# Kernel tuning notes

Hardware: AMD Instinct MI355X
Metric: run time of the kernel (lower is better)

The kernel has to match this reference:

```python
import jax, jax.numpy as jnp
import numpy as np
from jax import lax

# Static pair index table: all C(135,2)=9045 unordered node pairs (replaces the
# nested Python loops with a single gather).
PAIR_I, PAIR_J = np.triu_indices(135, k=1)
RRELU_SLOPE = (1.0 / 8.0 + 1.0 / 3.0) / 2.0  # eval-mode RReLU negative slope
BN_SCALE = 1.0 / float(np.sqrt(1.0 + 1e-5))  # eval BN with running mean=0, var=1


def _leaky(x):
    return jnp.where(x > 0, x, 0.01 * x)


def _conv1d(x, w, b):
    # x: (N, Cin, L), w: (Cout, Cin, K) -> (N, Cout, L-K+1), VALID
    y = lax.conv_general_dilated(x, w, (1,), 'VALID',
                                 dimension_numbers=('NCH', 'OIH', 'NCH'))
    return y + b[None, :, None]


def _bn_eval(x, g, b):
    # nn.BatchNorm1d in eval with fresh running stats (mean=0, var=1)
    return x * (g * BN_SCALE)[None, :, None] + b[None, :, None]


def _maxpool2d(x):
    # nn.MaxPool2d(2) applied to a 3D (N, H, W) tensor: 2x2 pool over (H, W)
    return lax.reduce_window(x, -jnp.inf, lax.max, (1, 2, 2), (1, 2, 2), 'VALID')


def setup_inputs() -> dict:
    key = jax.random.key(0)
    ks = iter(jax.random.split(key, 40))

    def w(shape, scale=0.05):
        return (jax.random.normal(next(ks), shape, jnp.float32) * scale)

    inp = {
        'x': jax.random.normal(next(ks), (30, 135, 375), jnp.float32),
        # FeatureExtractor
        'conv1_w': w((32, 1, 3)), 'conv1_b': jnp.zeros((32,), jnp.float32),
        'bn1_g': jnp.ones((32,), jnp.float32), 'bn1_b': jnp.zeros((32,), jnp.float32),
        'conv2_w': w((64, 16, 3)), 'conv2_b': jnp.zeros((64,), jnp.float32),
        'bn2_g': jnp.ones((64,), jnp.float32), 'bn2_b': jnp.zeros((64,), jnp.float32),
        'conv3_w': w((96, 32, 3)), 'conv3_b': jnp.zeros((96,), jnp.float32),
        'bn3_g': jnp.ones((96,), jnp.float32), 'bn3_b': jnp.zeros((96,), jnp.float32),
        'fe_fc_w': w((48 * 45, 32)), 'fe_fc_b': jnp.zeros((32,), jnp.float32),
        # SimilarityMeasureNetwork
        'sim_w1': w((64, 32)), 'sim_b1': jnp.zeros((32,), jnp.float32),
        'sim_w2': w((32, 16)), 'sim_b2': jnp.zeros((16,), jnp.float32),
        'sim_w3': w((16, 8)), 'sim_b3': jnp.zeros((8,), jnp.float32),
        'sim_w4': w((8, 1)), 'sim_b4': jnp.zeros((1,), jnp.float32),
        # ClassificationNet(9045, 3)
        'cls_w1': w((9045, 1024), 0.01), 'cls_b1': jnp.zeros((1024,), jnp.float32),
        'cls_w2': w((1024, 256)), 'cls_b2': jnp.zeros((256,), jnp.float32),
        'cls_w3': w((256, 64)), 'cls_b3': jnp.zeros((64,), jnp.float32),
        'cls_w4': w((64, 3)), 'cls_b4': jnp.zeros((3,), jnp.float32),
    }
    return inp


def reference(x, conv1_w, conv1_b, bn1_g, bn1_b, conv2_w, conv2_b, bn2_g, bn2_b,
              conv3_w, conv3_b, bn3_g, bn3_b, fe_fc_w, fe_fc_b,
              sim_w1, sim_b1, sim_w2, sim_b2, sim_w3, sim_b3, sim_w4, sim_b4,
              cls_w1, cls_b1, cls_w2, cls_b2, cls_w3, cls_b3, cls_w4, cls_b4):
    B = x.shape[0]  # 30 subjects
    h = x.reshape(B * 135, 1, 375)
    # FeatureExtractor (all subjects*nodes batched together)
    h = _maxpool2d(_leaky(_bn_eval(_conv1d(h, conv1_w, conv1_b), bn1_g, bn1_b)))  # (N,16,186)
    h = _maxpool2d(_leaky(_bn_eval(_conv1d(h, conv2_w, conv2_b), bn2_g, bn2_b)))  # (N,32,92)
    h = _maxpool2d(_leaky(_bn_eval(_conv1d(h, conv3_w, conv3_b), bn3_g, bn3_b)))  # (N,48,45)
    h = h.reshape(B * 135, -1) @ fe_fc_w + fe_fc_b  # (B*135, 32)
    feats = h.reshape(B, 135, 32)

    # All-pairs concat: single gather replacing the nested loops -> (B, 9045, 64)
    pi = jnp.asarray(PAIR_I)
    pj = jnp.asarray(PAIR_J)
    pairs = jnp.concatenate([feats[:, pi, :], feats[:, pj, :]], axis=-1)

    # SimilarityMeasureNetwork
    s = jax.nn.relu(pairs @ sim_w1 + sim_b1)
    s = jax.nn.relu(s @ sim_w2 + sim_b2)
    s = jax.nn.relu(s @ sim_w3 + sim_b3)
    s = jnp.tanh(s @ sim_w4 + sim_b4)  # (B, 9045, 1)
    subjects = s[..., 0]  # (B, 9045)

    # ClassificationNet (eval mode: RReLU -> fixed slope, dropout -> identity)
    c = subjects @ cls_w1 + cls_b1
    c = jnp.where(c >= 0, c, RRELU_SLOPE * c)
    c = jax.nn.relu(c @ cls_w2 + cls_b2)
    c = jax.nn.relu(c @ cls_w3 + cls_b3)
    c = c @ cls_w4 + cls_b4
    return jax.nn.log_softmax(c, axis=1)  # (B, 3)
```

## Files before the change

kernel.cpp:

```cpp
#include <hip/hip_runtime.h>
#include <math.h>

#define BN_SCALE 0.99999500003749967f
#define RRELU_SLOPE 0.22916666666666666f

static __device__ __forceinline__ float leaky(float v) { return v > 0.f ? v : 0.01f * v; }

typedef __attribute__((ext_vector_type(8))) short bf16x8;
typedef __attribute__((ext_vector_type(4))) float f32x4;

static __device__ __forceinline__ unsigned short f2bf(float f) {
  unsigned u = __builtin_bit_cast(unsigned, f);
  u = (u + 0x7FFFu + ((u >> 16) & 1u)) >> 16;
  return (unsigned short)u;
}

__global__ __launch_bounds__(256) void setup_kernel(
    const float* __restrict__ w2c, const float* __restrict__ g2,
    const float* __restrict__ w3c, const float* __restrict__ g3,
    const float* __restrict__ fcw, const float* __restrict__ fcb,
    const float* __restrict__ w1,  const float* __restrict__ b1,
    const float* __restrict__ cw1,
    unsigned short* __restrict__ w2frag,
    unsigned short* __restrict__ w3frag,
    unsigned short* __restrict__ bfragGG,
    float* __restrict__ bgagb,
    unsigned short* __restrict__ subjectsA,
    unsigned short* __restrict__ w1T)
{
  __shared__ float tile[64][65];
  const int t = threadIdx.x;
  if (blockIdx.x < 2272) {
    const int kt = blockIdx.x >> 4;
    const int ntb = blockIdx.x & 15;
    const int k0 = kt * 64, n0 = ntb * 64;
#pragma unroll 4
    for (int i = 0; i < 16; ++i) {
      const int idx = i * 256 + t;
      const int kk = idx >> 6, nn = idx & 63;
      const int k = k0 + kk;
      tile[kk][nn] = (k < 9045) ? cw1[(size_t)k * 1024 + n0 + nn] : 0.f;
    }
    __syncthreads();
#pragma unroll 4
    for (int i = 0; i < 8; ++i) {
      const int idx = i * 256 + t;
      const int nn = idx >> 5;
      const int kp = (idx & 31) * 2;
      const unsigned lo = f2bf(tile[kp][nn]);
      const unsigned hi = f2bf(tile[kp + 1][nn]);
      ((unsigned*)w1T)[(size_t)(n0 + nn) * 4544 + (k0 >> 1) + (idx & 31)] = lo | (hi << 16);
    }
    return;
  }
  const int item = (blockIdx.x - 2272) * 256 + t;
  if (item < 512) {
    const int tl = item >> 6, lane = item & 63;
    const int mt = tl >> 1, kc = tl & 1;
    const int lr = lane & 15, quad = lane >> 4;
    const int c = mt * 16 + lr;
    const float gs = g2[c] * BN_SCALE;
#pragma unroll
    for (int j = 0; j < 8; ++j) {
      const int k = quad * 8 + j;
      float v;
      if (kc == 0) { const int tap = k >> 4, ci = k & 15; v = w2c[c * 48 + ci * 3 + tap] * gs; }
      else         { v = (k < 16) ? w2c[c * 48 + k * 3 + 2] * gs : 0.f; }
      w2frag[item * 8 + j] = f2bf(v);
    }
  } else if (item < 1664) {
    const int it = item - 512;
    const int tl = it >> 6, lane = it & 63;
    const int mt = tl / 3, tap = tl - mt * 3;
    const int lr = lane & 15, quad = lane >> 4;
    const int c = mt * 16 + lr;
    const float gs = g3[c] * BN_SCALE;
#pragma unroll
    for (int j = 0; j < 8; ++j) {
      const int ci = quad * 8 + j;
      w3frag[it * 8 + j] = f2bf(w3c[c * 96 + ci * 3 + tap] * gs);
    }
  } else if (item < 19072) {
    const int it = item - 1664;
    const int chunk = it >> 8;
    const int rem = it & 255;
    const int nt = rem >> 6;
    const int lane = rem & 63;
    const int lr = lane & 15, quad = lane >> 4;
    const int n = nt * 16 + lr;
    const int off = (n >= 32) ? 32 : 0;
    const int nj = n & 31;
    float w1col[32];
#pragma unroll 8
    for (int q = 0; q < 32; ++q) w1col[q] = w1[(q + off) * 32 + nj];
#pragma unroll
    for (int j = 0; j < 8; ++j) {
      const int k = chunk * 32 + quad * 8 + j;
      float v = 0.f;
      if (k < 2160) {
        const float* fr = fcw + (size_t)k * 32;
#pragma unroll 8
        for (int q = 0; q < 32; ++q) v = fmaf(fr[q], w1col[q], v);
      }
      bfragGG[(size_t)it * 8 + j] = f2bf(v);
    }
  } else if (item < 19136) {
    const int n = item - 19072;
    const int off = (n >= 32) ? 32 : 0;
    const int nj = n & 31;
    float s = (n < 32) ? b1[nj] : 0.f;
    for (int q = 0; q < 32; ++q) s = fmaf(fcb[q], w1[(q + off) * 32 + nj], s);
    bgagb[n] = s;
  } else if (item < 55360) {
    const int idx = item - 19136;
    uint4 z = {0u, 0u, 0u, 0u};
    ((uint4*)subjectsA)[idx] = z;
  }
}

__global__ __launch_bounds__(128) void fe_kernel(
    const float* __restrict__ x,
    const float* __restrict__ w1c, const float* __restrict__ b1c,
    const float* __restrict__ g1,  const float* __restrict__ bb1,
    const float* __restrict__ b2c, const float* __restrict__ g2, const float* __restrict__ bb2,
    const float* __restrict__ b3c, const float* __restrict__ g3, const float* __restrict__ bb3,
    const unsigned short* __restrict__ w2frag,
    const unsigned short* __restrict__ w3frag,
    unsigned short* __restrict__ act3)
{
  __shared__ __align__(16) char smem[2 * 6912];
  const int t = threadIdx.x;
  const int wv = t >> 6, lane = t & 63, quad = lane >> 4, lr = lane & 15;
  const int n = blockIdx.x * 2 + wv;

  char* A = smem + wv * 6912;
  unsigned short* buf = (unsigned short*)A;
  float* be2 = (float*)(A + 6272);
  float* be3 = (float*)(A + 6528);

  bf16x8 a2[4][2];
#pragma unroll
  for (int mt = 0; mt < 4; ++mt)
#pragma unroll
    for (int kc = 0; kc < 2; ++kc)
      a2[mt][kc] = *(const bf16x8*)(w2frag + ((mt * 2 + kc) * 64 + lane) * 8);

  be2[lane] = b2c[lane] * (g2[lane] * BN_SCALE) + bb2[lane];
  be3[lane] = b3c[lane] * (g3[lane] * BN_SCALE) + bb3[lane];
  if (lane < 32) be3[64 + lane] = b3c[64 + lane] * (g3[64 + lane] * BN_SCALE) + bb3[64 + lane];
  ((unsigned*)buf)[1488 + lane] = 0;

  const int cp = lane & 7;
  float u[4][3], bbr[4];
#pragma unroll
  for (int d = 0; d < 4; ++d) {
    const int c = cp * 4 + d;
    const float gs = g1[c] * BN_SCALE;
    u[d][0] = w1c[c * 3 + 0] * gs;
    u[d][1] = w1c[c * 3 + 1] * gs;
    u[d][2] = w1c[c * 3 + 2] * gs;
    bbr[d] = b1c[c] * gs + bb1[c];
  }

  const float* xr = x + (size_t)n * 375;
  for (int o = lane; o < 1488; o += 64) {
    const int l = o >> 3;
    const int p = 2 * l;
    const float x0 = xr[p], x1 = xr[p + 1], x2 = xr[p + 2], x3 = xr[p + 3];
    unsigned pk = 0;
#pragma unroll
    for (int uu = 0; uu < 2; ++uu) {
      float m = -3.4e38f;
#pragma unroll
      for (int dc = 0; dc < 2; ++dc) {
        const int d = uu * 2 + dc;
        const float v0 = fmaf(x0, u[d][0], fmaf(x1, u[d][1], fmaf(x2, u[d][2], bbr[d])));
        const float v1 = fmaf(x1, u[d][0], fmaf(x2, u[d][1], fmaf(x3, u[d][2], bbr[d])));
        m = fmaxf(m, fmaxf(leaky(v0), leaky(v1)));
      }
      pk |= (unsigned)f2bf(m) << (16 * uu);
    }
    ((unsigned*)buf)[l * 8 + cp] = pk;
  }

  float be2r[4][4];
#pragma unroll
  for (int mt = 0; mt < 4; ++mt)
#pragma unroll
    for (int r = 0; r < 4; ++r) be2r[mt][r] = be2[mt * 16 + quad * 4 + r];

#pragma unroll 2
  for (int nt = 0; nt < 12; ++nt) {
    const int nrow = nt * 16 + lr;
    bf16x8 b0 = *(const bf16x8*)(buf + (nrow + (quad >> 1)) * 16 + (quad & 1) * 8);
    bf16x8 b1 = *(const bf16x8*)(buf + (nrow + 2) * 16 + (quad & 1) * 8);
    f32x4 acc[4];
#pragma unroll
    for (int mt = 0; mt < 4; ++mt)
#pragma unroll
      for (int r = 0; r < 4; ++r) acc[mt][r] = be2r[mt][r];
#pragma unroll
    for (int mt = 0; mt < 4; ++mt)
      acc[mt] = __builtin_amdgcn_mfma_f32_16x16x32_bf16(a2[mt][0], b0, acc[mt], 0, 0, 0);
#pragma unroll
    for (int mt = 0; mt < 4; ++mt)
      acc[mt] = __builtin_amdgcn_mfma_f32_16x16x32_bf16(a2[mt][1], b1, acc[mt], 0, 0, 0);
#pragma unroll
    for (int mt = 0; mt < 4; ++mt) {
      float o[4];
#pragma unroll
      for (int r = 0; r < 4; ++r) {
        const float v = leaky(acc[mt][r]);
        o[r] = fmaxf(v, __shfl_xor(v, 1));
      }
      if ((lr & 1) == 0) {
        const int np = nrow >> 1;
        if (np <= 91) {
          const float m0 = fmaxf(o[0], o[1]);
          const float m1 = fmaxf(o[2], o[3]);
          const unsigned pk = (unsigned)f2bf(m0) | ((unsigned)f2bf(m1) << 16);
          ((unsigned*)buf)[np * 16 + mt * 4 + quad] = pk;
        }
      }
    }
  }

  ((unsigned*)buf)[1472 + lane] = 0;
  if (lane < 32) ((unsigned*)buf)[1536 + lane] = 0;

  unsigned short* actr = act3 + (size_t)n * 2176;
  for (int mt = 0; mt < 6; ++mt) {
    bf16x8 a3[3];
#pragma unroll
    for (int tap = 0; tap < 3; ++tap)
      a3[tap] = *(const bf16x8*)(w3frag + ((mt * 3 + tap) * 64 + lane) * 8);
    float be3r[4];
#pragma unroll
    for (int r = 0; r < 4; ++r) be3r[r] = be3[mt * 16 + quad * 4 + r];
#pragma unroll
    for (int nt = 0; nt < 6; ++nt) {
      const int nrow = nt * 16 + lr;
      f32x4 acc;
#pragma unroll
      for (int r = 0; r < 4; ++r) acc[r] = be3r[r];
#pragma unroll
      for (int tap = 0; tap < 3; ++tap) {
        bf16x8 b = *(const bf16x8*)(buf + (nrow + tap) * 32 + quad * 8);
        acc = __builtin_amdgcn_mfma_f32_16x16x32_bf16(a3[tap], b, acc, 0, 0, 0);
      }
      float o[4];
#pragma unroll
      for (int r = 0; r < 4; ++r) {
        const float v = leaky(acc[r]);
        o[r] = fmaxf(v, __shfl_xor(v, 1));
      }
      if ((lr & 1) == 0) {
        const int np = nrow >> 1;
        if (np <= 44) {
          const int mp = mt * 8 + quad * 2;
          actr[mp * 45 + np] = f2bf(fmaxf(o[0], o[1]));
          actr[(mp + 1) * 45 + np] = f2bf(fmaxf(o[2], o[3]));
        }
      }
    }
  }
  if (lane < 16) actr[2160 + lane] = 0;
}

__global__ __launch_bounds__(256) void gagb_kernel(
    const unsigned short* __restrict__ act3,
    const unsigned short* __restrict__ bfragGG,
    const float* __restrict__ bgagb,
    float* __restrict__ Ga, float* __restrict__ Gb)
{
  __shared__ f32x4 sred[3][4][64];
  const int t = threadIdx.x;
  const int wv = t >> 6, lane = t & 63, quad = lane >> 4, lr = lane & 15;
  const int m0 = blockIdx.x * 16;
  const int arow = min(m0 + lr, 4049);

  f32x4 acc[4] = {};
  const int c0 = wv * 17;
  for (int chunk = c0; chunk < c0 + 17; ++chunk) {
    const bf16x8 a = *(const bf16x8*)(act3 + (size_t)arow * 2176 + chunk * 32 + quad * 8);
#pragma unroll
    for (int nt = 0; nt < 4; ++nt) {
      const bf16x8 b = *(const bf16x8*)(bfragGG + ((size_t)(chunk * 4 + nt) * 64 + lane) * 8);
      acc[nt] = __builtin_amdgcn_mfma_f32_16x16x32_bf16(a, b, acc[nt], 0, 0, 0);
    }
  }
  if (wv > 0) {
#pragma unroll
    for (int nt = 0; nt < 4; ++nt) sred[wv - 1][nt][lane] = acc[nt];
  }
  __syncthreads();
  if (wv == 0) {
#pragma unroll
    for (int nt = 0; nt < 4; ++nt) {
      f32x4 s = acc[nt];
#pragma unroll
      for (int q = 0; q < 3; ++q) {
        const f32x4 o = sred[q][nt][lane];
#pragma unroll
        for (int r = 0; r < 4; ++r) s[r] += o[r];
      }
      const int col = nt * 16 + lr;
      const float bias = bgagb[col];
#pragma unroll
      for (int r = 0; r < 4; ++r) {
        const int row = m0 + quad * 4 + r;
        if (row < 4050) {
          const float v = s[r] + bias;
          if (col < 32) Ga[row * 32 + col] = v;
          else          Gb[row * 32 + (col - 32)] = v;
        }
      }
    }
  }
}

__global__ __launch_bounds__(256) void sim_kernel(
    const float* __restrict__ Ga, const float* __restrict__ Gb,
    const float* __restrict__ w2, const float* __restrict__ b2,
    const float* __restrict__ w3, const float* __restrict__ b3,
    const float* __restrict__ w4, const float* __restrict__ b4,
    unsigned short* __restrict__ subjectsA)
{
  __shared__ float sGa[135 * 36];
  __shared__ float sGb[135 * 36];
  __shared__ float sw2[512], sw3[128], sw4[8];
  __shared__ float sb2[16], sb3[8], sb4v[1];

  const int t = threadIdx.x;
  const int b = blockIdx.x >> 5;
  const int c = blockIdx.x & 31;

  for (int i = t; i < 4320; i += 256) {
    const int r = i >> 5, col = i & 31;
    sGa[r * 36 + col] = Ga[b * 4320 + i];
    sGb[r * 36 + col] = Gb[b * 4320 + i];
  }
  for (int i = t; i < 512; i += 256) sw2[i] = w2[i];
  if (t < 128) sw3[t] = w3[t];
  if (t < 8) sw4[t] = w4[t];
  if (t < 16) sb2[t] = b2[t];
  if (t < 8) sb3[t] = b3[t];
  if (t == 0) sb4v[0] = b4[0];
  __syncthreads();

  const int mtile = b >> 4, lrm = b & 15;
  const int pend = min(9045, (c + 1) * 283);
  for (int p = c * 283 + t; p < pend; p += 256) {
    int i = (int)((269.0f - sqrtf((float)(72361 - 8 * p))) * 0.5f);
    i = max(0, min(133, i));
    while (134 * (i + 1) - ((i + 1) * i) / 2 <= p) ++i;
    while (134 * i - (i * (i - 1)) / 2 > p) --i;
    const int j = i + 1 + (p - (134 * i - (i * (i - 1)) / 2));

    float h1[32];
#pragma unroll
    for (int q = 0; q < 8; ++q) {
      const float4 va = *(const float4*)(&sGa[i * 36 + 4 * q]);
      const float4 vb = *(const float4*)(&sGb[j * 36 + 4 * q]);
      h1[4 * q + 0] = fmaxf(va.x + vb.x, 0.f);
      h1[4 * q + 1] = fmaxf(va.y + vb.y, 0.f);
      h1[4 * q + 2] = fmaxf(va.z + vb.z, 0.f);
      h1[4 * q + 3] = fmaxf(va.w + vb.w, 0.f);
    }

    float h2[16];
#pragma unroll
    for (int jj = 0; jj < 16; ++jj) h2[jj] = sb2[jj];
#pragma unroll 8
    for (int ii = 0; ii < 32; ++ii) {
      const float av = h1[ii];
      const float4* wr = reinterpret_cast<const float4*>(&sw2[ii * 16]);
#pragma unroll
      for (int r = 0; r < 4; ++r) {
        float4 w = wr[r];
        h2[4 * r + 0] = fmaf(av, w.x, h2[4 * r + 0]);
        h2[4 * r + 1] = fmaf(av, w.y, h2[4 * r + 1]);
        h2[4 * r + 2] = fmaf(av, w.z, h2[4 * r + 2]);
        h2[4 * r + 3] = fmaf(av, w.w, h2[4 * r + 3]);
      }
    }
#pragma unroll
    for (int jj = 0; jj < 16; ++jj) h2[jj] = fmaxf(h2[jj], 0.f);

    float h3[8];
#pragma unroll
    for (int jj = 0; jj < 8; ++jj) h3[jj] = sb3[jj];
#pragma unroll
    for (int ii = 0; ii < 16; ++ii) {
      const float av = h2[ii];
      const float4* wr = reinterpret_cast<const float4*>(&sw3[ii * 8]);
#pragma unroll
      for (int r = 0; r < 2; ++r) {
        float4 w = wr[r];
        h3[4 * r + 0] = fmaf(av, w.x, h3[4 * r + 0]);
        h3[4 * r + 1] = fmaf(av, w.y, h3[4 * r + 1]);
        h3[4 * r + 2] = fmaf(av, w.z, h3[4 * r + 2]);
        h3[4 * r + 3] = fmaf(av, w.w, h3[4 * r + 3]);
      }
    }
#pragma unroll
    for (int jj = 0; jj < 8; ++jj) h3[jj] = fmaxf(h3[jj], 0.f);

    float z = sb4v[0];
#pragma unroll
    for (int ii = 0; ii < 8; ++ii) z = fmaf(h3[ii], sw4[ii], z);

    const float az = fabsf(z);
    const float e = __expf(-2.f * az);
    const float rr = (1.f - e) / (1.f + e);
    const float val = copysignf(rr, z);

    const int chunk = p >> 5, q8 = (p & 31) >> 3, jj2 = p & 7;
    subjectsA[chunk * 1024 + mtile * 512 + (q8 * 16 + lrm) * 8 + jj2] = f2bf(val);
  }
}

__global__ __launch_bounds__(256) void c1_kernel(
    const unsigned short* __restrict__ subjectsA,
    const unsigned short* __restrict__ w1T,
    float* __restrict__ part)
{
  const int t = threadIdx.x;
  const int wv = t >> 6, lane = t & 63, quad = lane >> 4, lr = lane & 15;
  const int job = blockIdx.x * 4 + wv;
  const int ng = job & 15;
  const int kg = job >> 4;
  const int c0 = kg * 5;
  const int cend = min(283, c0 + 5);

  f32x4 acc[2][4] = {};
  for (int ch = c0; ch < cend; ++ch) {
    const bf16x8 a0 = *(const bf16x8*)(subjectsA + ch * 1024 + lane * 8);
    const bf16x8 a1 = *(const bf16x8*)(subjectsA + ch * 1024 + 512 + lane * 8);
#pragma unroll
    for (int nt = 0; nt < 4; ++nt) {
      const int col = (ng * 4 + nt) * 16 + lr;
      const bf16x8 b = *(const bf16x8*)(w1T + (size_t)col * 9088 + ch * 32 + quad * 8);
      acc[0][nt] = __builtin_amdgcn_mfma_f32_16x16x32_bf16(a0, b, acc[0][nt], 0, 0, 0);
      acc[1][nt] = __builtin_amdgcn_mfma_f32_16x16x32_bf16(a1, b, acc[1][nt], 0, 0, 0);
    }
  }
#pragma unroll
  for (int mt = 0; mt < 2; ++mt)
#pragma unroll
    for (int r = 0; r < 4; ++r) {
      const int m = mt * 16 + quad * 4 + r;
      if (m < 30) {
#pragma unroll
        for (int nt = 0; nt < 4; ++nt) {
          const int col = (ng * 4 + nt) * 16 + lr;
          part[(size_t)(m * 64 + kg) * 1024 + col] = acc[mt][nt][r];
        }
      }
    }
}

__global__ __launch_bounds__(256) void tail_a_kernel(
    const float* __restrict__ part,
    const float* __restrict__ cb1,
    float* __restrict__ act1)
{
  const int r = blockIdx.x >> 2;
  const int cg = blockIdx.x & 3;
  const int j = cg * 256 + threadIdx.x;
  float s = cb1[j];
  const float* pp = part + (size_t)r * 64 * 1024 + j;
#pragma unroll 8
  for (int q = 0; q < 64; ++q) s += pp[q * 1024];
  act1[r * 1024 + j] = s >= 0.f ? s : RRELU_SLOPE * s;
}

__global__ __launch_bounds__(256) void tail_b_kernel(
    const float* __restrict__ act1,
    const float* __restrict__ w2, const float* __restrict__ cb2,
    float* __restrict__ act2)
{
  __shared__ float sa[1024];
  __shared__ float sp[256];
  const int r = blockIdx.x >> 3;
  const int cg = blockIdx.x & 7;
  const int t = threadIdx.x;
  const int c = t & 31;
  const int ks = t >> 5;
  const int col = cg * 32 + c;

  for (int i = t; i < 1024; i += 256) sa[i] = act1[r * 1024 + i];
  __syncthreads();

  float acc = 0.f;
  const int k0 = ks * 128;
  for (int kk = k0; kk < k0 + 128; kk += 4) {
    const float4 a = *reinterpret_cast<const float4*>(&sa[kk]);
    acc = fmaf(a.x, w2[(kk + 0) * 256 + col], acc);
    acc = fmaf(a.y, w2[(kk + 1) * 256 + col], acc);
    acc = fmaf(a.z, w2[(kk + 2) * 256 + col], acc);
    acc = fmaf(a.w, w2[(kk + 3) * 256 + col], acc);
  }
  sp[t] = acc;
  __syncthreads();
  if (t < 32) {
    float s = cb2[col];
#pragma unroll
    for (int q = 0; q < 8; ++q) s += sp[q * 32 + t];
    act2[r * 256 + cg * 32 + t] = fmaxf(s, 0.f);
  }
}

__global__ __launch_bounds__(256) void tail_c_kernel(
    const float* __restrict__ act2,
    const float* __restrict__ w3, const float* __restrict__ cb3,
    const float* __restrict__ w4, const float* __restrict__ cb4,
    float* __restrict__ out)
{
  __shared__ float sa[256];
  __shared__ float sp[256];
  __shared__ float sc3[64];
  __shared__ float slg[3];
  const int r = blockIdx.x, t = threadIdx.x;
  const int c = t & 63;
  const int ks = t >> 6;

  sa[t] = act2[r * 256 + t];
  __syncthreads();
  {
    float acc = 0.f;
    const int k0 = ks * 64;
#pragma unroll 4
    for (int kk = k0; kk < k0 + 64; ++kk)
      acc = fmaf(sa[kk], w3[kk * 64 + c], acc);
    sp[t] = acc;
  }
  __syncthreads();
  if (t < 64) {
    const float s = cb3[t] + sp[t] + sp[t + 64] + sp[t + 128] + sp[t + 192];
    sc3[t] = fmaxf(s, 0.f);
  }
  __syncthreads();
  if (t < 3) {
    float acc = cb4[t];
#pragma unroll
    for (int kk = 0; kk < 64; ++kk) acc = fmaf(sc3[kk], w4[kk * 3 + t], acc);
    slg[t] = acc;
  }
  __syncthreads();
  if (t == 0) {
    float m = fmaxf(slg[0], fmaxf(slg[1], slg[2]));
    float se = __expf(slg[0] - m) + __expf(slg[1] - m) + __expf(slg[2] - m);
    float lse = m + logf(se);
    out[r * 3 + 0] = slg[0] - lse;
    out[r * 3 + 1] = slg[1] - lse;
    out[r * 3 + 2] = slg[2] - lse;
  }
}

extern "C" void kernel_launch(void* const* d_in, const int* in_sizes, int n_in,
                              void* d_out, int out_size, void* d_ws, size_t ws_size,
                              hipStream_t stream) {
  const float* x    = (const float*)d_in[0];
  const float* w1c  = (const float*)d_in[1];
  const float* b1c  = (const float*)d_in[2];
  const float* g1   = (const float*)d_in[3];
  const float* bb1  = (const float*)d_in[4];
  const float* w2c  = (const float*)d_in[5];
  const float* b2c  = (const float*)d_in[6];
  const float* g2   = (const float*)d_in[7];
  const float* bb2  = (const float*)d_in[8];
  const float* w3c  = (const float*)d_in[9];
  const float* b3c  = (const float*)d_in[10];
  const float* g3   = (const float*)d_in[11];
  const float* bb3  = (const float*)d_in[12];
  const float* fcw  = (const float*)d_in[13];
  const float* fcb  = (const float*)d_in[14];
  const float* sw1  = (const float*)d_in[15];
  const float* sb1  = (const float*)d_in[16];
  const float* sw2  = (const float*)d_in[17];
  const float* sb2  = (const float*)d_in[18];
  const float* sw3  = (const float*)d_in[19];
  const float* sb3  = (const float*)d_in[20];
  const float* sw4  = (const float*)d_in[21];
  const float* sb4  = (const float*)d_in[22];
  const float* cw1  = (const float*)d_in[23];
  const float* cb1  = (const float*)d_in[24];
  const float* cw2  = (const float*)d_in[25];
  const float* cb2  = (const float*)d_in[26];
  const float* cw3  = (const float*)d_in[27];
  const float* cb3  = (const float*)d_in[28];
  const float* cw4  = (const float*)d_in[29];
  const float* cb4  = (const float*)d_in[30];

  float* ws = (float*)d_ws;
  float* Ga    = ws;
  float* Gb    = ws + 129600;
  float* part  = ws + 259200;
  float* bgagb = ws + 2225280;
  float* act1  = ws + 2225344;
  float* act2  = ws + 2256064;
  unsigned short* wsu = (unsigned short*)(ws + 2263744);
  unsigned short* w2frag    = wsu;
  unsigned short* w3frag    = wsu + 4096;
  unsigned short* bfragGG   = wsu + 13312;
  unsigned short* act3      = wsu + 152576;
  unsigned short* subjectsA = wsu + 8965376;
  unsigned short* w1T       = wsu + 9255168;

  setup_kernel<<<2489, 256, 0, stream>>>(w2c, g2, w3c, g3, fcw, fcb, sw1, sb1, cw1,
                                         w2frag, w3frag, bfragGG, bgagb, subjectsA, w1T);
  fe_kernel<<<2025, 128, 0, stream>>>(x, w1c, b1c, g1, bb1, b2c, g2, bb2,
                                      b3c, g3, bb3, w2frag, w3frag, act3);
  gagb_kernel<<<254, 256, 0, stream>>>(act3, bfragGG, bgagb, Ga, Gb);
  sim_kernel<<<960, 256, 0, stream>>>(Ga, Gb, sw2, sb2, sw3, sb3, sw4, sb4, subjectsA);
  c1_kernel<<<256, 256, 0, stream>>>(subjectsA, w1T, part);
  tail_a_kernel<<<120, 256, 0, stream>>>(part, cb1, act1);
  tail_b_kernel<<<240, 256, 0, stream>>>(act1, cw2, cb2, act2);
  tail_c_kernel<<<30, 256, 0, stream>>>(act2, cw3, cb3, cw4, cb4, (float*)d_out);
}
```

Measured before the change: 270.5 us.

## Merge setup and feature extractor, atomically reduce classifier partials, fuse tail kernels

New measurement: 315.6 us. 16.7% more time.

```diff
diff --git a/kernel.cpp b/kernel.cpp
--- a/kernel.cpp
+++ b/kernel.cpp
@@ -15,24 +15,194 @@
   return (unsigned short)u;
 }
 
-__global__ __launch_bounds__(256) void setup_kernel(
-    const float* __restrict__ w2c, const float* __restrict__ g2,
-    const float* __restrict__ w3c, const float* __restrict__ g3,
+__global__ __launch_bounds__(256) void big_kernel(
+    const float* __restrict__ x,
+    const float* __restrict__ w1c, const float* __restrict__ b1c,
+    const float* __restrict__ g1,  const float* __restrict__ bb1,
+    const float* __restrict__ w2c, const float* __restrict__ b2c,
+    const float* __restrict__ g2,  const float* __restrict__ bb2,
+    const float* __restrict__ w3c, const float* __restrict__ b3c,
+    const float* __restrict__ g3,  const float* __restrict__ bb3,
     const float* __restrict__ fcw, const float* __restrict__ fcb,
     const float* __restrict__ w1,  const float* __restrict__ b1,
-    const float* __restrict__ cw1,
-    unsigned short* __restrict__ w2frag,
-    unsigned short* __restrict__ w3frag,
+    const float* __restrict__ cw1, const float* __restrict__ cb1,
+    unsigned short* __restrict__ act3,
     unsigned short* __restrict__ bfragGG,
     float* __restrict__ bgagb,
     unsigned short* __restrict__ subjectsA,
-    unsigned short* __restrict__ w1T)
+    unsigned short* __restrict__ w1T,
+    float* __restrict__ act1pre)
 {
-  __shared__ float tile[64][65];
+  __shared__ __align__(16) char smem[27648];
   const int t = threadIdx.x;
-  if (blockIdx.x < 2272) {
-    const int kt = blockIdx.x >> 4;
-    const int ntb = blockIdx.x & 15;
+
+  if (blockIdx.x < 1013) {
+    const int wv = t >> 6, lane = t & 63, quad = lane >> 4, lr = lane & 15;
+    const int n = blockIdx.x * 4 + wv;
+    if (n >= 4050) return;
+
+    char* A = smem + wv * 6912;
+    unsigned short* buf = (unsigned short*)A;
+    float* be2 = (float*)(A + 6272);
+    float* be3 = (float*)(A + 6528);
+
+    bf16x8 a2[4][2];
+#pragma unroll
+    for (int mt = 0; mt < 4; ++mt) {
+      const int c = mt * 16 + lr;
+      const float gs = g2[c] * BN_SCALE;
+#pragma unroll
+      for (int kc = 0; kc < 2; ++kc) {
+        bf16x8 fr;
+#pragma unroll
+        for (int j = 0; j < 8; ++j) {
+          const int k = quad * 8 + j;
+          float v;
+          if (kc == 0) { const int tap = k >> 4, ci = k & 15; v = w2c[c * 48 + ci * 3 + tap] * gs; }
+          else         { v = (k < 16) ? w2c[c * 48 + k * 3 + 2] * gs : 0.f; }
+          fr[j] = (short)f2bf(v);
+        }
+        a2[mt][kc] = fr;
+      }
+    }
+
+    be2[lane] = b2c[lane] * (g2[lane] * BN_SCALE) + bb2[lane];
+    be3[lane] = b3c[lane] * (g3[lane] * BN_SCALE) + bb3[lane];
+    if (lane < 32) be3[64 + lane] = b3c[64 + lane] * (g3[64 + lane] * BN_SCALE) + bb3[64 + lane];
+    ((unsigned*)buf)[1488 + lane] = 0;
+
+    const int cp = lane & 7;
+    float u[4][3], bbr[4];
+#pragma unroll
+    for (int d = 0; d < 4; ++d) {
+      const int c = cp * 4 + d;
+      const float gs = g1[c] * BN_SCALE;
+      u[d][0] = w1c[c * 3 + 0] * gs;
+      u[d][1] = w1c[c * 3 + 1] * gs;
+      u[d][2] = w1c[c * 3 + 2] * gs;
+      bbr[d] = b1c[c] * gs + bb1[c];
+    }
+
+    const float* xr = x + (size_t)n * 375;
+    for (int o = lane; o < 1488; o += 64) {
+      const int l = o >> 3;
+      const int p = 2 * l;
+      const float x0 = xr[p], x1 = xr[p + 1], x2 = xr[p + 2], x3 = xr[p + 3];
+      unsigned pk = 0;
+#pragma unroll
+      for (int uu = 0; uu < 2; ++uu) {
+        float m = -3.4e38f;
+#pragma unroll
+        for (int dc = 0; dc < 2; ++dc) {
+          const int d = uu * 2 + dc;
+          const float v0 = fmaf(x0, u[d][0], fmaf(x1, u[d][1], fmaf(x2, u[d][2], bbr[d])));
+          const float v1 = fmaf(x1, u[d][0], fmaf(x2, u[d][1], fmaf(x3, u[d][2], bbr[d])));
+          m = fmaxf(m, fmaxf(leaky(v0), leaky(v1)));
+        }
+        pk |= (unsigned)f2bf(m) << (16 * uu);
+      }
+      ((unsigned*)buf)[l * 8 + cp] = pk;
+    }
+
+    float be2r[4][4];
+#pragma unroll
+    for (int mt = 0; mt < 4; ++mt)
+#pragma unroll
+      for (int r = 0; r < 4; ++r) be2r[mt][r] = be2[mt * 16 + quad * 4 + r];
+
+#pragma unroll 2
+    for (int nt = 0; nt < 12; ++nt) {
+      const int nrow = nt * 16 + lr;
+      bf16x8 b0 = *(const bf16x8*)(buf + (nrow + (quad >> 1)) * 16 + (quad & 1) * 8);
+      bf16x8 b1 = *(const bf16x8*)(buf + (nrow + 2) * 16 + (quad & 1) * 8);
+      f32x4 acc[4];
+#pragma unroll
+      for (int mt = 0; mt < 4; ++mt)
+#pragma unroll
+        for (int r = 0; r < 4; ++r) acc[mt][r] = be2r[mt][r];
+#pragma unroll
+      for (int mt = 0; mt < 4; ++mt)
+        acc[mt] = __builtin_amdgcn_mfma_f32_16x16x32_bf16(a2[mt][0], b0, acc[mt], 0, 0, 0);
+#pragma unroll
+      for (int mt = 0; mt < 4; ++mt)
+        acc[mt] = __builtin_amdgcn_mfma_f32_16x16x32_bf16(a2[mt][1], b1, acc[mt], 0, 0, 0);
+#pragma unroll
+      for (int mt = 0; mt < 4; ++mt) {
+        float o[4];
+#pragma unroll
+        for (int r = 0; r < 4; ++r) {
+          const float v = leaky(acc[mt][r]);
+          o[r] = fmaxf(v, __shfl_xor(v, 1));
+        }
+        if ((lr & 1) == 0) {
+          const int np = nrow >> 1;
+          if (np <= 91) {
+            const float m0 = fmaxf(o[0], o[1]);
+            const float m1 = fmaxf(o[2], o[3]);
+            const unsigned pk = (unsigned)f2bf(m0) | ((unsigned)f2bf(m1) << 16);
+            ((unsigned*)buf)[np * 16 + mt * 4 + quad] = pk;
+          }
+        }
+      }
+    }
+
+    ((unsigned*)buf)[1472 + lane] = 0;
+    if (lane < 32) ((unsigned*)buf)[1536 + lane] = 0;
+
+    unsigned short* actr = act3 + (size_t)n * 2176;
+    for (int mt = 0; mt < 6; ++mt) {
+      const int c = mt * 16 + lr;
+      const float gs3v = g3[c] * BN_SCALE;
+      bf16x8 a3[3];
+#pragma unroll
+      for (int tap = 0; tap < 3; ++tap) {
+        bf16x8 fr;
+#pragma unroll
+        for (int j = 0; j < 8; ++j) {
+          const int ci = quad * 8 + j;
+          fr[j] = (short)f2bf(w3c[c * 96 + ci * 3 + tap] * gs3v);
+        }
+        a3[tap] = fr;
+      }
+      float be3r[4];
+#pragma unroll
+      for (int r = 0; r < 4; ++r) be3r[r] = be3[mt * 16 + quad * 4 + r];
+#pragma unroll
+      for (int nt = 0; nt < 6; ++nt) {
+        const int nrow = nt * 16 + lr;
+        f32x4 acc;
+#pragma unroll
+        for (int r = 0; r < 4; ++r) acc[r] = be3r[r];
+#pragma unroll
+        for (int tap = 0; tap < 3; ++tap) {
+          bf16x8 b = *(const bf16x8*)(buf + (nrow + tap) * 32 + quad * 8);
+          acc = __builtin_amdgcn_mfma_f32_16x16x32_bf16(a3[tap], b, acc, 0, 0, 0);
+        }
+        float o[4];
+#pragma unroll
+        for (int r = 0; r < 4; ++r) {
+          const float v = leaky(acc[r]);
+          o[r] = fmaxf(v, __shfl_xor(v, 1));
+        }
+        if ((lr & 1) == 0) {
+          const int np = nrow >> 1;
+          if (np <= 44) {
+            const int mp = mt * 8 + quad * 2;
+            actr[mp * 45 + np] = f2bf(fmaxf(o[0], o[1]));
+            actr[(mp + 1) * 45 + np] = f2bf(fmaxf(o[2], o[3]));
+          }
+        }
+      }
+    }
+    if (lane < 16) actr[2160 + lane] = 0;
+    return;
+  }
+
+  const int sb = blockIdx.x - 1013;
+  if (sb < 2272) {
+    float (*tile)[65] = (float(*)[65])smem;
+    const int kt = sb >> 4;
+    const int ntb = sb & 15;
     const int k0 = kt * 64, n0 = ntb * 64;
 #pragma unroll 4
     for (int i = 0; i < 16; ++i) {
@@ -53,43 +223,17 @@
     }
     return;
   }
-  const int item = (blockIdx.x - 2272) * 256 + t;
-  if (item < 512) {
-    const int tl = item >> 6, lane = item & 63;
-    const int mt = tl >> 1, kc = tl & 1;
-    const int lr = lane & 15, quad = lane >> 4;
-    const int c = mt * 16 + lr;
-    const float gs = g2[c] * BN_SCALE;
-#pragma unroll
-    for (int j = 0; j < 8; ++j) {
-      const int k = quad * 8 + j;
-      float v;
-      if (kc == 0) { const int tap = k >> 4, ci = k & 15; v = w2c[c * 48 + ci * 3 + tap] * gs; }
-      else         { v = (k < 16) ? w2c[c * 48 + k * 3 + 2] * gs : 0.f; }
-      w2frag[item * 8 + j] = f2bf(v);
-    }
-  } else if (item < 1664) {
-    const int it = item - 512;
-    const int tl = it >> 6, lane = it & 63;
-    const int mt = tl / 3, tap = tl - mt * 3;
-    const int lr = lane & 15, quad = lane >> 4;
-    const int c = mt * 16 + lr;
-    const float gs = g3[c] * BN_SCALE;
-#pragma unroll
-    for (int j = 0; j < 8; ++j) {
-      const int ci = quad * 8 + j;
-      w3frag[it * 8 + j] = f2bf(w3c[c * 96 + ci * 3 + tap] * gs);
-    }
-  } else if (item < 19072) {
-    const int it = item - 1664;
-    const int chunk = it >> 8;
-    const int rem = it & 255;
+
+  const int item = (sb - 2272) * 256 + t;
+  if (item < 17408) {
+    const int chunk = item >> 8;
+    const int rem = item & 255;
     const int nt = rem >> 6;
     const int lane = rem & 63;
     const int lr = lane & 15, quad = lane >> 4;
-    const int n = nt * 16 + lr;
-    const int off = (n >= 32) ? 32 : 0;
-    const int nj = n & 31;
+    const int nn = nt * 16 + lr;
+    const int off = (nn >= 32) ? 32 : 0;
+    const int nj = nn & 31;
     float w1col[32];
 #pragma unroll 8
     for (int q = 0; q < 32; ++q) w1col[q] = w1[(q + off) * 32 + nj];
@@ -102,169 +246,25 @@
 #pragma unroll 8
         for (int q = 0; q < 32; ++q) v = fmaf(fr[q], w1col[q], v);
       }
-      bfragGG[(size_t)it * 8 + j] = f2bf(v);
-    }
-  } else if (item < 19136) {
-    const int n = item - 19072;
-    const int off = (n >= 32) ? 32 : 0;
-    const int nj = n & 31;
-    float s = (n < 32) ? b1[nj] : 0.f;
+      bfragGG[(size_t)item * 8 + j] = f2bf(v);
+    }
+  } else if (item < 17472) {
+    const int nn = item - 17408;
+    const int off = (nn >= 32) ? 32 : 0;
+    const int nj = nn & 31;
+    float s = (nn < 32) ? b1[nj] : 0.f;
     for (int q = 0; q < 32; ++q) s = fmaf(fcb[q], w1[(q + off) * 32 + nj], s);
-    bgagb[n] = s;
-  } else if (item < 55360) {
-    const int idx = item - 19136;
+    bgagb[nn] = s;
+  } else if (item < 53696) {
+    const int idx = item - 17472;
     uint4 z = {0u, 0u, 0u, 0u};
     ((uint4*)subjectsA)[idx] = z;
-  }
-}
-
-__global__ __launch_bounds__(128) void fe_kernel(
-    const float* __restrict__ x,
-    const float* __restrict__ w1c, const float* __restrict__ b1c,
-    const float* __restrict__ g1,  const float* __restrict__ bb1,
-    const float* __restrict__ b2c, const float* __restrict__ g2, const float* __restrict__ bb2,
-    const float* __restrict__ b3c, const float* __restrict__ g3, const float* __restrict__ bb3,
-    const unsigned short* __restrict__ w2frag,
-    const unsigned short* __restrict__ w3frag,
-    unsigned short* __restrict__ act3)
-{
-  __shared__ __align__(16) char smem[2 * 6912];
-  const int t = threadIdx.x;
-  const int wv = t >> 6, lane = t & 63, quad = lane >> 4, lr = lane & 15;
-  const int n = blockIdx.x * 2 + wv;
-
-  char* A = smem + wv * 6912;
-  unsigned short* buf = (unsigned short*)A;
-  float* be2 = (float*)(A + 6272);
-  float* be3 = (float*)(A + 6528);
-
-  bf16x8 a2[4][2];
-#pragma unroll
-  for (int mt = 0; mt < 4; ++mt)
-#pragma unroll
-    for (int kc = 0; kc < 2; ++kc)
-      a2[mt][kc] = *(const bf16x8*)(w2frag + ((mt * 2 + kc) * 64 + lane) * 8);
-
-  be2[lane] = b2c[lane] * (g2[lane] * BN_SCALE) + bb2[lane];
-  be3[lane] = b3c[lane] * (g3[lane] * BN_SCALE) + bb3[lane];
-  if (lane < 32) be3[64 + lane] = b3c[64 + lane] * (g3[64 + lane] * BN_SCALE) + bb3[64 + lane];
-  ((unsigned*)buf)[1488 + lane] = 0;
-
-  const int cp = lane & 7;
-  float u[4][3], bbr[4];
-#pragma unroll
-  for (int d = 0; d < 4; ++d) {
-    const int c = cp * 4 + d;
-    const float gs = g1[c] * BN_SCALE;
-    u[d][0] = w1c[c * 3 + 0] * gs;
-    u[d][1] = w1c[c * 3 + 1] * gs;
-    u[d][2] = w1c[c * 3 + 2] * gs;
-    bbr[d] = b1c[c] * gs + bb1[c];
-  }
-
-  const float* xr = x + (size_t)n * 375;
-  for (int o = lane; o < 1488; o += 64) {
-    const int l = o >> 3;
-    const int p = 2 * l;
-    const float x0 = xr[p], x1 = xr[p + 1], x2 = xr[p + 2], x3 = xr[p + 3];
-    unsigned pk = 0;
-#pragma unroll
-    for (int uu = 0; uu < 2; ++uu) {
-      float m = -3.4e38f;
-#pragma unroll
-      for (int dc = 0; dc < 2; ++dc) {
-        const int d = uu * 2 + dc;
-        const float v0 = fmaf(x0, u[d][0], fmaf(x1, u[d][1], fmaf(x2, u[d][2], bbr[d])));
-        const float v1 = fmaf(x1, u[d][0], fmaf(x2, u[d][1], fmaf(x3, u[d][2], bbr[d])));
-        m = fmaxf(m, fmaxf(leaky(v0), leaky(v1)));
-      }
-      pk |= (unsigned)f2bf(m) << (16 * uu);
-    }
-    ((unsigned*)buf)[l * 8 + cp] = pk;
-  }
-
-  float be2r[4][4];
-#pragma unroll
-  for (int mt = 0; mt < 4; ++mt)
-#pragma unroll
-    for (int r = 0; r < 4; ++r) be2r[mt][r] = be2[mt * 16 + quad * 4 + r];
-
-#pragma unroll 2
-  for (int nt = 0; nt < 12; ++nt) {
-    const int nrow = nt * 16 + lr;
-    bf16x8 b0 = *(const bf16x8*)(buf + (nrow + (quad >> 1)) * 16 + (quad & 1) * 8);
-    bf16x8 b1 = *(const bf16x8*)(buf + (nrow + 2) * 16 + (quad & 1) * 8);
-    f32x4 acc[4];
-#pragma unroll
-    for (int mt = 0; mt < 4; ++mt)
-#pragma unroll
-      for (int r = 0; r < 4; ++r) acc[mt][r] = be2r[mt][r];
-#pragma unroll
-    for (int mt = 0; mt < 4; ++mt)
-      acc[mt] = __builtin_amdgcn_mfma_f32_16x16x32_bf16(a2[mt][0], b0, acc[mt], 0, 0, 0);
-#pragma unroll
-    for (int mt = 0; mt < 4; ++mt)
-      acc[mt] = __builtin_amdgcn_mfma_f32_16x16x32_bf16(a2[mt][1], b1, acc[mt], 0, 0, 0);
-#pragma unroll
-    for (int mt = 0; mt < 4; ++mt) {
-      float o[4];
-#pragma unroll
-      for (int r = 0; r < 4; ++r) {
-        const float v = leaky(acc[mt][r]);
-        o[r] = fmaxf(v, __shfl_xor(v, 1));
-      }
-      if ((lr & 1) == 0) {
-        const int np = nrow >> 1;
-        if (np <= 91) {
-          const float m0 = fmaxf(o[0], o[1]);
-          const float m1 = fmaxf(o[2], o[3]);
-          const unsigned pk = (unsigned)f2bf(m0) | ((unsigned)f2bf(m1) << 16);
-          ((unsigned*)buf)[np * 16 + mt * 4 + quad] = pk;
-        }
-      }
-    }
-  }
-
-  ((unsigned*)buf)[1472 + lane] = 0;
-  if (lane < 32) ((unsigned*)buf)[1536 + lane] = 0;
-
-  unsigned short* actr = act3 + (size_t)n * 2176;
-  for (int mt = 0; mt < 6; ++mt) {
-    bf16x8 a3[3];
-#pragma unroll
-    for (int tap = 0; tap < 3; ++tap)
-      a3[tap] = *(const bf16x8*)(w3frag + ((mt * 3 + tap) * 64 + lane) * 8);
-    float be3r[4];
-#pragma unroll
-    for (int r = 0; r < 4; ++r) be3r[r] = be3[mt * 16 + quad * 4 + r];
-#pragma unroll
-    for (int nt = 0; nt < 6; ++nt) {
-      const int nrow = nt * 16 + lr;
-      f32x4 acc;
-#pragma unroll
-      for (int r = 0; r < 4; ++r) acc[r] = be3r[r];
-#pragma unroll
-      for (int tap = 0; tap < 3; ++tap) {
-        bf16x8 b = *(const bf16x8*)(buf + (nrow + tap) * 32 + quad * 8);
-        acc = __builtin_amdgcn_mfma_f32_16x16x32_bf16(a3[tap], b, acc, 0, 0, 0);
-      }
-      float o[4];
-#pragma unroll
-      for (int r = 0; r < 4; ++r) {
-        const float v = leaky(acc[r]);
-        o[r] = fmaxf(v, __shfl_xor(v, 1));
-      }
-      if ((lr & 1) == 0) {
-        const int np = nrow >> 1;
-        if (np <= 44) {
-          const int mp = mt * 8 + quad * 2;
-          actr[mp * 45 + np] = f2bf(fmaxf(o[0], o[1]));
-          actr[(mp + 1) * 45 + np] = f2bf(fmaxf(o[2], o[3]));
-        }
-      }
-    }
-  }
-  if (lane < 16) actr[2160 + lane] = 0;
+  } else if (item < 61376) {
+    const int idx = item - 53696;
+    const int r = idx >> 8, q = idx & 255;
+    const float4 v = *(const float4*)(cb1 + q * 4);
+    *(float4*)(act1pre + (size_t)r * 1024 + q * 4) = v;
+  }
 }
 
 __global__ __launch_bounds__(256) void gagb_kernel(
@@ -423,7 +423,7 @@
 __global__ __launch_bounds__(256) void c1_kernel(
     const unsigned short* __restrict__ subjectsA,
     const unsigned short* __restrict__ w1T,
-    float* __restrict__ part)
+    float* __restrict__ act1pre)
 {
   const int t = threadIdx.x;
   const int wv = t >> 6, lane = t & 63, quad = lane >> 4, lr = lane & 15;
@@ -454,90 +454,61 @@
 #pragma unroll
         for (int nt = 0; nt < 4; ++nt) {
           const int col = (ng * 4 + nt) * 16 + lr;
-          part[(size_t)(m * 64 + kg) * 1024 + col] = acc[mt][nt][r];
-        }
-      }
-    }
-}
-
-__global__ __launch_bounds__(256) void tail_a_kernel(
-    const float* __restrict__ part,
-    const float* __restrict__ cb1,
-    float* __restrict__ act1)
-{
-  const int r = blockIdx.x >> 2;
-  const int cg = blockIdx.x & 3;
-  const int j = cg * 256 + threadIdx.x;
-  float s = cb1[j];
-  const float* pp = part + (size_t)r * 64 * 1024 + j;
-#pragma unroll 8
-  for (int q = 0; q < 64; ++q) s += pp[q * 1024];
-  act1[r * 1024 + j] = s >= 0.f ? s : RRELU_SLOPE * s;
-}
-
-__global__ __launch_bounds__(256) void tail_b_kernel(
-    const float* __restrict__ act1,
+          atomicAdd(&act1pre[(size_t)m * 1024 + col], acc[mt][nt][r]);
+        }
+      }
+    }
+}
+
+__global__ __launch_bounds__(1024) void tail_kernel(
+    const float* __restrict__ act1pre,
     const float* __restrict__ w2, const float* __restrict__ cb2,
-    float* __restrict__ act2)
-{
-  __shared__ float sa[1024];
-  __shared__ float sp[256];
-  const int r = blockIdx.x >> 3;
-  const int cg = blockIdx.x & 7;
-  const int t = threadIdx.x;
-  const int c = t & 31;
-  const int ks = t >> 5;
-  const int col = cg * 32 + c;
-
-  for (int i = t; i < 1024; i += 256) sa[i] = act1[r * 1024 + i];
-  __syncthreads();
-
-  float acc = 0.f;
-  const int k0 = ks * 128;
-  for (int kk = k0; kk < k0 + 128; kk += 4) {
-    const float4 a = *reinterpret_cast<const float4*>(&sa[kk]);
-    acc = fmaf(a.x, w2[(kk + 0) * 256 + col], acc);
-    acc = fmaf(a.y, w2[(kk + 1) * 256 + col], acc);
-    acc = fmaf(a.z, w2[(kk + 2) * 256 + col], acc);
-    acc = fmaf(a.w, w2[(kk + 3) * 256 + col], acc);
-  }
-  sp[t] = acc;
-  __syncthreads();
-  if (t < 32) {
-    float s = cb2[col];
-#pragma unroll
-    for (int q = 0; q < 8; ++q) s += sp[q * 32 + t];
-    act2[r * 256 + cg * 32 + t] = fmaxf(s, 0.f);
-  }
-}
-
-__global__ __launch_bounds__(256) void tail_c_kernel(
-    const float* __restrict__ act2,
     const float* __restrict__ w3, const float* __restrict__ cb3,
     const float* __restrict__ w4, const float* __restrict__ cb4,
     float* __restrict__ out)
 {
-  __shared__ float sa[256];
-  __shared__ float sp[256];
+  __shared__ float sc1[1024];
+  __shared__ float sp[1024];
+  __shared__ float sact2[256];
   __shared__ float sc3[64];
   __shared__ float slg[3];
   const int r = blockIdx.x, t = threadIdx.x;
-  const int c = t & 63;
-  const int ks = t >> 6;
-
-  sa[t] = act2[r * 256 + t];
-  __syncthreads();
+
   {
+    const float s = act1pre[(size_t)r * 1024 + t];
+    sc1[t] = s >= 0.f ? s : RRELU_SLOPE * s;
+  }
+  __syncthreads();
+  {
+    const int col = t & 255, ks = t >> 8;
     float acc = 0.f;
-    const int k0 = ks * 64;
+    const int k0 = ks * 256;
+    for (int kk = k0; kk < k0 + 256; kk += 4) {
+      const float4 a = *reinterpret_cast<const float4*>(&sc1[kk]);
+      acc = fmaf(a.x, w2[(kk + 0) * 256 + col], acc);
+      acc = fmaf(a.y, w2[(kk + 1) * 256 + col], acc);
+      acc = fmaf(a.z, w2[(kk + 2) * 256 + col], acc);
+      acc = fmaf(a.w, w2[(kk + 3) * 256 + col], acc);
+    }
+    sp[t] = acc;
+  }
+  __syncthreads();
+  if (t < 256) sact2[t] = fmaxf(cb2[t] + sp[t] + sp[t + 256] + sp[t + 512] + sp[t + 768], 0.f);
+  __syncthreads();
+  {
+    const int col = t & 63, ks = t >> 6;
+    float acc = 0.f;
+    const int k0 = ks * 16;
 #pragma unroll 4
-    for (int kk = k0; kk < k0 + 64; ++kk)
-      acc = fmaf(sa[kk], w3[kk * 64 + c], acc);
+    for (int kk = k0; kk < k0 + 16; ++kk)
+      acc = fmaf(sact2[kk], w3[kk * 64 + col], acc);
     sp[t] = acc;
   }
   __syncthreads();
   if (t < 64) {
-    const float s = cb3[t] + sp[t] + sp[t + 64] + sp[t + 128] + sp[t + 192];
+    float s = cb3[t];
+#pragma unroll
+    for (int q = 0; q < 16; ++q) s += sp[q * 64 + t];
     sc3[t] = fmaxf(s, 0.f);
   }
   __syncthreads();
@@ -549,9 +520,9 @@
   }
   __syncthreads();
   if (t == 0) {
-    float m = fmaxf(slg[0], fmaxf(slg[1], slg[2]));
-    float se = __expf(slg[0] - m) + __expf(slg[1] - m) + __expf(slg[2] - m);
-    float lse = m + logf(se);
+    const float m = fmaxf(slg[0], fmaxf(slg[1], slg[2]));
+    const float se = __expf(slg[0] - m) + __expf(slg[1] - m) + __expf(slg[2] - m);
+    const float lse = m + logf(se);
     out[r * 3 + 0] = slg[0] - lse;
     out[r * 3 + 1] = slg[1] - lse;
     out[r * 3 + 2] = slg[2] - lse;
@@ -594,28 +565,22 @@
   const float* cb4  = (const float*)d_in[30];
 
   float* ws = (float*)d_ws;
-  float* Ga    = ws;
-  float* Gb    = ws + 129600;
-  float* part  = ws + 259200;
-  float* bgagb = ws + 2225280;
-  float* act1  = ws + 2225344;
-  float* act2  = ws + 2256064;
-  unsigned short* wsu = (unsigned short*)(ws + 2263744);
-  unsigned short* w2frag    = wsu;
-  unsigned short* w3frag    = wsu + 4096;
-  unsigned short* bfragGG   = wsu + 13312;
-  unsigned short* act3      = wsu + 152576;
-  unsigned short* subjectsA = wsu + 8965376;
-  unsigned short* w1T       = wsu + 9255168;
-
-  setup_kernel<<<2489, 256, 0, stream>>>(w2c, g2, w3c, g3, fcw, fcb, sw1, sb1, cw1,
-                                         w2frag, w3frag, bfragGG, bgagb, subjectsA, w1T);
-  fe_kernel<<<2025, 128, 0, stream>>>(x, w1c, b1c, g1, bb1, b2c, g2, bb2,
-                                      b3c, g3, bb3, w2frag, w3frag, act3);
+  float* Ga      = ws;
+  float* Gb      = ws + 129600;
+  float* bgagb   = ws + 259200;
+  float* act1pre = ws + 259264;
+  unsigned short* wsu = (unsigned short*)(ws + 289984);
+  unsigned short* bfragGG   = wsu;
+  unsigned short* act3      = wsu + 139264;
+  unsigned short* subjectsA = wsu + 8952064;
+  unsigned short* w1T       = wsu + 9241856;
+
+  big_kernel<<<3525, 256, 0, stream>>>(x, w1c, b1c, g1, bb1, w2c, b2c, g2, bb2,
+                                       w3c, b3c, g3, bb3, fcw, fcb, sw1, sb1,
+                                       cw1, cb1, act3, bfragGG, bgagb,
+                                       subjectsA, w1T, act1pre);
   gagb_kernel<<<254, 256, 0, stream>>>(act3, bfragGG, bgagb, Ga, Gb);
   sim_kernel<<<960, 256, 0, stream>>>(Ga, Gb, sw2, sb2, sw3, sb3, sw4, sb4, subjectsA);
-  c1_kernel<<<256, 256, 0, stream>>>(subjectsA, w1T, part);
-  tail_a_kernel<<<120, 256, 0, stream>>>(part, cb1, act1);
-  tail_b_kernel<<<240, 256, 0, stream>>>(act1, cw2, cb2, act2);
-  tail_c_kernel<<<30, 256, 0, stream>>>(act2, cw3, cb3, cw4, cb4, (float*)d_out);
-}
+  c1_kernel<<<256, 256, 0, stream>>>(subjectsA, w1T, act1pre);
+  tail_kernel<<<30, 1024, 0, stream>>>(act1pre, cw2, cb2, cw3, cb3, cw4, cb4, (float*)d_out);
+}
```
